# Kernel tuning notes

Hardware: AMD Instinct MI355X
Metric: run time of the kernel (lower is better)

## Reference

```python
import jax, jax.numpy as jnp
import numpy as np

DIM = 768
HEADS = 12
HEAD_DIM = DIM // HEADS
SCALE = HEAD_DIM ** -0.5


def setup_inputs() -> dict:
    key = jax.random.key(0)
    ks = jax.random.split(key, 7)
    B, N, C = 4, 1024, DIM
    s = 0.02
    return {
        "x": jax.random.normal(ks[0], (B, N, C), dtype=jnp.float32),
        "attn_mask": jax.random.normal(ks[1], (B, N, N), dtype=jnp.float32) * 0.1,
        "w_qkv": jax.random.normal(ks[2], (3 * C, C), dtype=jnp.float32) * s,
        "w_proj": jax.random.normal(ks[3], (C, C), dtype=jnp.float32) * s,
        "b_proj": jnp.zeros((C,), dtype=jnp.float32),
        "w_pre": jax.random.normal(ks[4], (HEADS, HEADS), dtype=jnp.float32) * 0.2,
        "w_post": jax.random.normal(ks[5], (HEADS, HEADS), dtype=jnp.float32) * 0.2,
    }


def reference(x, attn_mask, w_qkv, w_proj, b_proj, w_pre, w_post):
    B, N, C = x.shape
    H, D = HEADS, HEAD_DIM
    qkv = (x @ w_qkv.T).reshape(B, N, 3, H, D)
    q, k, v = jnp.moveaxis(qkv, 2, 0)          # each [B, N, H, D]
    q = q.transpose(0, 2, 1, 3)                # [B, H, N, D]
    k = k.transpose(0, 2, 1, 3)
    v = v.transpose(0, 2, 1, 3)
    attn = jnp.einsum("bhnd,bhmd->bhnm", q, k) * SCALE
    attn = attn + attn_mask[:, None, :, :]
    # talking-heads pre-softmax mixing: Linear over head axis (y = x @ W.T)
    attn = jnp.einsum("bhnm,gh->bgnm", attn, w_pre)
    attn = jax.nn.softmax(attn, axis=-1)
    # talking-heads post-softmax mixing
    attn = jnp.einsum("bhnm,gh->bgnm", attn, w_post)
    out = jnp.einsum("bhnm,bhmd->bhnd", attn, v)   # [B, H, N, D]
    out = out.transpose(0, 2, 1, 3).reshape(B, N, C)
    return out @ w_proj.T + b_proj
```

## Files before the change

kernel.cpp:

```cpp
#include <hip/hip_runtime.h>
#include <hip/hip_bf16.h>

typedef __attribute__((ext_vector_type(8))) short bf16x8;
typedef __attribute__((ext_vector_type(4))) float f32x4;
typedef unsigned short u16;

#define ATT_SCALE 0.125f

__device__ __forceinline__ u16 f2bf(float f){
  __hip_bfloat16 h = __float2bfloat16(f);
  return *reinterpret_cast<u16*>(&h);
}
__device__ __forceinline__ float bf2f(u16 u){
  __hip_bfloat16 h;
  *reinterpret_cast<u16*>(&h) = u;
  return __bfloat162float(h);
}

__global__ __launch_bounds__(256) void cvt_kernel(const float* __restrict__ src,
                                                  u16* __restrict__ dst, int n4){
  int i = blockIdx.x*256 + threadIdx.x;
  if (i < n4){
    float4 v = reinterpret_cast<const float4*>(src)[i];
    ushort4 o;
    o.x = f2bf(v.x); o.y = f2bf(v.y); o.z = f2bf(v.z); o.w = f2bf(v.w);
    reinterpret_cast<ushort4*>(dst)[i] = o;
  }
}

template<int BM, int BN, int MODE>
__global__ __launch_bounds__(256) void gemm_bt(
    const u16* __restrict__ A, const u16* __restrict__ B,
    void* __restrict__ C0, void* __restrict__ C1, void* __restrict__ C2,
    const float* __restrict__ bias,
    int M, int N, int K, int lda, int ldb, long sA, long sB, long sC)
{
  constexpr int BK = 32, LDT = 40;
  __shared__ u16 As[BM*LDT];
  __shared__ u16 Bs[BN*LDT];
  const int z = blockIdx.z;
  const u16* Ab = A + (long)z * sA;
  const u16* Bb = B + (long)z * sB;
  const int bm = blockIdx.x * BM, bn = blockIdx.y * BN;
  const int tid = threadIdx.x, lane = tid & 63, wv = tid >> 6;
  constexpr int WM = BM/2, WN = BN/2, FM = WM/16, FN = WN/16;
  const int wm = (wv >> 1) * WM, wn = (wv & 1) * WN;
  const int quad = lane >> 4, cl = lane & 15;
  f32x4 acc[FM][FN];
  #pragma unroll
  for (int i=0;i<FM;i++)
    #pragma unroll
    for (int j=0;j<FN;j++){ f32x4 zr = {0.f,0.f,0.f,0.f}; acc[i][j] = zr; }
  constexpr int AIT = (BM*BK)/(8*256);
  constexpr int BIT = (BN*BK)/(8*256);

  for (int kb = 0; kb < K; kb += BK){
    __syncthreads();
    #pragma unroll
    for (int sL=0; sL<AIT; sL++){
      int e = tid + sL*256, r = e >> 2, c8 = (e & 3) * 8;
      *reinterpret_cast<float4*>(&As[r*LDT + c8]) =
        *reinterpret_cast<const float4*>(Ab + (long)(bm + r)*lda + kb + c8);
    }
    #pragma unroll
    for (int sL=0; sL<BIT; sL++){
      int e = tid + sL*256, r = e >> 2, c8 = (e & 3) * 8;
      *reinterpret_cast<float4*>(&Bs[r*LDT + c8]) =
        *reinterpret_cast<const float4*>(Bb + (long)(bn + r)*ldb + kb + c8);
    }
    __syncthreads();
    bf16x8 af[FM], bfr[FN];
    #pragma unroll
    for (int i=0;i<FM;i++)
      af[i] = *reinterpret_cast<const bf16x8*>(&As[(wm + i*16 + cl)*LDT + quad*8]);
    #pragma unroll
    for (int j=0;j<FN;j++)
      bfr[j] = *reinterpret_cast<const bf16x8*>(&Bs[(wn + j*16 + cl)*LDT + quad*8]);
    #pragma unroll
    for (int i=0;i<FM;i++)
      #pragma unroll
      for (int j=0;j<FN;j++)
        acc[i][j] = __builtin_amdgcn_mfma_f32_16x16x32_bf16(af[i], bfr[j], acc[i][j], 0, 0, 0);
  }

  #pragma unroll
  for (int i=0;i<FM;i++)
  #pragma unroll
  for (int j=0;j<FN;j++)
  #pragma unroll
  for (int r=0;r<4;r++){
    int gm = bm + wm + i*16 + quad*4 + r;
    int gn = bn + wn + j*16 + cl;
    float v = acc[i][j][r];
    if (MODE == 0){
      int b_ = gm >> 10, n_ = gm & 1023;
      int t3 = (gn >= 1536) ? 2 : ((gn >= 768) ? 1 : 0);
      int rem = gn - t3*768;
      int h = rem >> 6, d = rem & 63;
      u16 hv = f2bf(v);
      if (t3 == 0)      ((u16*)C0)[((long)((b_*12 + h)*1024 + n_))*64 + d] = hv;
      else if (t3 == 1) ((u16*)C1)[((long)((b_*12 + h)*1024 + n_))*64 + d] = hv;
      else              ((u16*)C2)[((long)((b_*12 + h)*64 + d))*1024 + n_] = hv;
    } else if (MODE == 1){
      ((u16*)C0)[(long)z*sC + (long)gm*N + gn] = f2bf(v);
    } else if (MODE == 2){
      int b_ = z / 12, h = z - b_*12;
      ((u16*)C0)[((long)((b_*1024 + gm)*12 + h))*64 + gn] = f2bf(v);
    } else {
      ((float*)C0)[(long)gm*N + gn] = v + bias[gn];
    }
  }
}

__global__ __launch_bounds__(256) void mix_kernel(
    u16* __restrict__ S, const float* __restrict__ mask,
    const float* __restrict__ w_pre, const float* __restrict__ w_post)
{
  const int bid = blockIdx.x;
  const int b = bid >> 10, n = bid & 1023;
  const int t = threadIdx.x, wv = t >> 6, lane = t & 63;
  const int m0 = t * 4;

  float s[12][4];
  #pragma unroll
  for (int h=0; h<12; h++){
    ushort4 v = *reinterpret_cast<const ushort4*>(
        S + ((long)((b*12 + h)*1024 + n))*1024 + m0);
    s[h][0]=bf2f(v.x); s[h][1]=bf2f(v.y); s[h][2]=bf2f(v.z); s[h][3]=bf2f(v.w);
  }
  float4 mk = *reinterpret_cast<const float4*>(mask + ((long)(b*1024 + n))*1024 + m0);
  float mkv[4] = {mk.x, mk.y, mk.z, mk.w};

  float smix[12][4];
  #pragma unroll
  for (int g=0; g<12; g++){
    float rs = 0.f;
    #pragma unroll
    for (int h=0; h<12; h++) rs += w_pre[g*12 + h];
    #pragma unroll
    for (int mi=0; mi<4; mi++) smix[g][mi] = rs * mkv[mi];
    #pragma unroll
    for (int h=0; h<12; h++){
      float w = w_pre[g*12 + h] * ATT_SCALE;
      #pragma unroll
      for (int mi=0; mi<4; mi++) smix[g][mi] += w * s[h][mi];
    }
  }

  __shared__ float redA[12][4];
  __shared__ float redB[12][4];
  float Mg[12];
  #pragma unroll
  for (int g=0; g<12; g++){
    float v = fmaxf(fmaxf(smix[g][0], smix[g][1]), fmaxf(smix[g][2], smix[g][3]));
    #pragma unroll
    for (int off=32; off>0; off>>=1) v = fmaxf(v, __shfl_xor(v, off));
    if (lane == 0) redA[g][wv] = v;
  }
  __syncthreads();
  #pragma unroll
  for (int g=0; g<12; g++)
    Mg[g] = fmaxf(fmaxf(redA[g][0], redA[g][1]), fmaxf(redA[g][2], redA[g][3]));

  #pragma unroll
  for (int g=0; g<12; g++){
    float sum = 0.f;
    #pragma unroll
    for (int mi=0; mi<4; mi++){
      float e = __expf(smix[g][mi] - Mg[g]);
      smix[g][mi] = e; sum += e;
    }
    #pragma unroll
    for (int off=32; off>0; off>>=1) sum += __shfl_xor(sum, off);
    if (lane == 0) redB[g][wv] = sum;
  }
  __syncthreads();
  #pragma unroll
  for (int g=0; g<12; g++){
    float L = redB[g][0] + redB[g][1] + redB[g][2] + redB[g][3];
    float inv = 1.f / L;
    #pragma unroll
    for (int mi=0; mi<4; mi++) smix[g][mi] *= inv;
  }

  #pragma unroll
  for (int h=0; h<12; h++){
    float o0=0.f,o1=0.f,o2=0.f,o3=0.f;
    #pragma unroll
    for (int g=0; g<12; g++){
      float w = w_post[h*12 + g];
      o0 += w*smix[g][0]; o1 += w*smix[g][1]; o2 += w*smix[g][2]; o3 += w*smix[g][3];
    }
    ushort4 st; st.x=f2bf(o0); st.y=f2bf(o1); st.z=f2bf(o2); st.w=f2bf(o3);
    *reinterpret_cast<ushort4*>(S + ((long)((b*12 + h)*1024 + n))*1024 + m0) = st;
  }
}

extern "C" void kernel_launch(void* const* d_in, const int* in_sizes, int n_in,
                              void* d_out, int out_size, void* d_ws, size_t ws_size,
                              hipStream_t stream)
{
  const float* x      = (const float*)d_in[0];
  const float* mask   = (const float*)d_in[1];
  const float* w_qkv  = (const float*)d_in[2];
  const float* w_proj = (const float*)d_in[3];
  const float* b_proj = (const float*)d_in[4];
  const float* w_pre  = (const float*)d_in[5];
  const float* w_post = (const float*)d_in[6];
  float* out = (float*)d_out;

  u16* xb     = (u16*)d_ws;
  u16* wqkvb  = xb     + 4096l*768;
  u16* wprojb = wqkvb  + 2304l*768;
  u16* Qb     = wprojb + 768l*768;
  u16* Kb     = Qb     + 48l*1024*64;
  u16* Vtb    = Kb     + 48l*1024*64;
  u16* tmpb   = Vtb    + 48l*1024*64;
  u16* Sb     = tmpb   + 4096l*768;
  size_t need = ((size_t)(Sb - xb) + 48ul*1024*1024) * sizeof(u16);
  if (ws_size < need) return;

  cvt_kernel<<<(4096*768/4 + 255)/256, 256, 0, stream>>>(x,      xb,     4096*768/4);
  cvt_kernel<<<(2304*768/4 + 255)/256, 256, 0, stream>>>(w_qkv,  wqkvb,  2304*768/4);
  cvt_kernel<<<(768*768/4  + 255)/256, 256, 0, stream>>>(w_proj, wprojb, 768*768/4);

  dim3 gq(4096/128, 2304/128, 1);
  gemm_bt<128,128,0><<<gq, 256, 0, stream>>>(xb, wqkvb, Qb, Kb, Vtb, nullptr,
      4096, 2304, 768, 768, 768, 0, 0, 0);

  dim3 gs(1024/128, 1024/128, 48);
  gemm_bt<128,128,1><<<gs, 256, 0, stream>>>(Qb, Kb, Sb, nullptr, nullptr, nullptr,
      1024, 1024, 64, 64, 64, 1024l*64, 1024l*64, 1024l*1024);

  mix_kernel<<<4096, 256, 0, stream>>>(Sb, mask, w_pre, w_post);

  dim3 gp(1024/128, 1, 48);
  gemm_bt<128,64,2><<<gp, 256, 0, stream>>>(Sb, Vtb, tmpb, nullptr, nullptr, nullptr,
      1024, 64, 1024, 1024, 1024, 1024l*1024, 64l*1024, 0);

  dim3 go(4096/128, 768/128, 1);
  gemm_bt<128,128,3><<<go, 256, 0, stream>>>(tmpb, wprojb, out, nullptr, nullptr, b_proj,
      4096, 768, 768, 768, 768, 0, 0, 0);
}
```

Baseline: 275.8 us.

## Do talking-heads mixing with MFMA and drop the softmax max pass

```diff
diff --git a/kernel.cpp b/kernel.cpp
--- a/kernel.cpp
+++ b/kernel.cpp
@@ -4,6 +4,7 @@
 typedef __attribute__((ext_vector_type(8))) short bf16x8;
 typedef __attribute__((ext_vector_type(4))) float f32x4;
 typedef unsigned short u16;
+typedef unsigned int u32;
 
 #define ATT_SCALE 0.125f
 
@@ -112,87 +113,113 @@
   }
 }
 
-__global__ __launch_bounds__(256) void mix_kernel(
+#define SMP 1032
+
+__global__ __launch_bounds__(256) void mix2_kernel(
     u16* __restrict__ S, const float* __restrict__ mask,
     const float* __restrict__ w_pre, const float* __restrict__ w_post)
 {
+  __shared__ u16 Sh[12*SMP];
+  __shared__ float maskS[1024];
+  __shared__ float Lred[4][16];
+  __shared__ float LinvS[16];
+
   const int bid = blockIdx.x;
   const int b = bid >> 10, n = bid & 1023;
   const int t = threadIdx.x, wv = t >> 6, lane = t & 63;
-  const int m0 = t * 4;
-
-  float s[12][4];
-  #pragma unroll
-  for (int h=0; h<12; h++){
-    ushort4 v = *reinterpret_cast<const ushort4*>(
-        S + ((long)((b*12 + h)*1024 + n))*1024 + m0);
-    s[h][0]=bf2f(v.x); s[h][1]=bf2f(v.y); s[h][2]=bf2f(v.z); s[h][3]=bf2f(v.w);
-  }
-  float4 mk = *reinterpret_cast<const float4*>(mask + ((long)(b*1024 + n))*1024 + m0);
-  float mkv[4] = {mk.x, mk.y, mk.z, mk.w};
-
-  float smix[12][4];
-  #pragma unroll
-  for (int g=0; g<12; g++){
-    float rs = 0.f;
-    #pragma unroll
-    for (int h=0; h<12; h++) rs += w_pre[g*12 + h];
-    #pragma unroll
-    for (int mi=0; mi<4; mi++) smix[g][mi] = rs * mkv[mi];
-    #pragma unroll
-    for (int h=0; h<12; h++){
-      float w = w_pre[g*12 + h] * ATT_SCALE;
+  const int quad = lane >> 4, cl = lane & 15;
+
+  #pragma unroll
+  for (int it = 0; it < 6; it++){
+    int idx = t + it*256;
+    int h = idx >> 7, m = (idx & 127)*8;
+    *reinterpret_cast<float4*>(&Sh[h*SMP + m]) =
+      *reinterpret_cast<const float4*>(S + ((long)((b*12 + h)*1024 + n))*1024 + m);
+  }
+  for (int i = t; i < 1024; i += 256)
+    maskS[i] = mask[((long)(b*1024 + n))*1024 + i];
+
+  float rs_[4];
+  #pragma unroll
+  for (int r = 0; r < 4; r++){
+    int g = quad*4 + r;
+    float v = 0.f;
+    if (g < 12)
+      for (int h = 0; h < 12; h++) v += w_pre[g*12 + h];
+    rs_[r] = v;
+  }
+  union FragU { bf16x8 v; u32 u[4]; u16 s[8]; };
+  FragU a_pre;
+  #pragma unroll
+  for (int j = 0; j < 8; j++){
+    int k = quad*8 + j;
+    a_pre.s[j] = (cl < 12 && k < 12) ? f2bf(w_pre[cl*12 + k] * ATT_SCALE) : (u16)0;
+  }
+  __syncthreads();
+
+  u32 Ep01[16], Ep23[16];
+  float Lacc[4] = {0.f, 0.f, 0.f, 0.f};
+  const f32x4 zero4 = {0.f, 0.f, 0.f, 0.f};
+
+  #pragma unroll
+  for (int j = 0; j < 16; j++){
+    int mcol = (wv*16 + j)*16 + cl;
+    FragU bs;
+    #pragma unroll
+    for (int jj = 0; jj < 8; jj++){
+      int hh = quad*8 + jj;
+      bs.s[jj] = (hh < 12) ? Sh[hh*SMP + mcol] : (u16)0;
+    }
+    f32x4 d = __builtin_amdgcn_mfma_f32_16x16x32_bf16(a_pre.v, bs.v, zero4, 0, 0, 0);
+    float mval = maskS[mcol];
+    float e0 = __expf(d[0] + rs_[0]*mval);
+    float e1 = __expf(d[1] + rs_[1]*mval);
+    float e2 = __expf(d[2] + rs_[2]*mval);
+    float e3 = __expf(d[3] + rs_[3]*mval);
+    Lacc[0] += e0; Lacc[1] += e1; Lacc[2] += e2; Lacc[3] += e3;
+    Ep01[j] = (u32)f2bf(e0) | ((u32)f2bf(e1) << 16);
+    Ep23[j] = (u32)f2bf(e2) | ((u32)f2bf(e3) << 16);
+  }
+
+  #pragma unroll
+  for (int r = 0; r < 4; r++){
+    float v = Lacc[r];
+    v += __shfl_xor(v, 1); v += __shfl_xor(v, 2);
+    v += __shfl_xor(v, 4); v += __shfl_xor(v, 8);
+    Lacc[r] = v;
+  }
+  if (cl == 0){
+    #pragma unroll
+    for (int r = 0; r < 4; r++) Lred[wv][quad*4 + r] = Lacc[r];
+  }
+  __syncthreads();
+  if (t < 16) LinvS[t] = 1.f / (Lred[0][t] + Lred[1][t] + Lred[2][t] + Lred[3][t]);
+  __syncthreads();
+
+  FragU a_post;
+  #pragma unroll
+  for (int j = 0; j < 8; j++){
+    int k = quad*8 + j;
+    a_post.s[j] = (cl < 12 && k < 12) ? f2bf(w_post[cl*12 + k] * LinvS[k]) : (u16)0;
+  }
+
+  const int srcA = (quad << 5) + cl;
+  #pragma unroll
+  for (int j = 0; j < 16; j++){
+    int mcol = (wv*16 + j)*16 + cl;
+    FragU be;
+    be.u[0] = (u32)__shfl((int)Ep01[j], srcA, 64);
+    be.u[1] = (u32)__shfl((int)Ep23[j], srcA, 64);
+    be.u[2] = (u32)__shfl((int)Ep01[j], srcA + 16, 64);
+    be.u[3] = (u32)__shfl((int)Ep23[j], srcA + 16, 64);
+    f32x4 d = __builtin_amdgcn_mfma_f32_16x16x32_bf16(a_post.v, be.v, zero4, 0, 0, 0);
+    if (quad < 3){
       #pragma unroll
-      for (int mi=0; mi<4; mi++) smix[g][mi] += w * s[h][mi];
-    }
-  }
-
-  __shared__ float redA[12][4];
-  __shared__ float redB[12][4];
-  float Mg[12];
-  #pragma unroll
-  for (int g=0; g<12; g++){
-    float v = fmaxf(fmaxf(smix[g][0], smix[g][1]), fmaxf(smix[g][2], smix[g][3]));
-    #pragma unroll
-    for (int off=32; off>0; off>>=1) v = fmaxf(v, __shfl_xor(v, off));
-    if (lane == 0) redA[g][wv] = v;
-  }
-  __syncthreads();
-  #pragma unroll
-  for (int g=0; g<12; g++)
-    Mg[g] = fmaxf(fmaxf(redA[g][0], redA[g][1]), fmaxf(redA[g][2], redA[g][3]));
-
-  #pragma unroll
-  for (int g=0; g<12; g++){
-    float sum = 0.f;
-    #pragma unroll
-    for (int mi=0; mi<4; mi++){
-      float e = __expf(smix[g][mi] - Mg[g]);
-      smix[g][mi] = e; sum += e;
-    }
-    #pragma unroll
-    for (int off=32; off>0; off>>=1) sum += __shfl_xor(sum, off);
-    if (lane == 0) redB[g][wv] = sum;
-  }
-  __syncthreads();
-  #pragma unroll
-  for (int g=0; g<12; g++){
-    float L = redB[g][0] + redB[g][1] + redB[g][2] + redB[g][3];
-    float inv = 1.f / L;
-    #pragma unroll
-    for (int mi=0; mi<4; mi++) smix[g][mi] *= inv;
-  }
-
-  #pragma unroll
-  for (int h=0; h<12; h++){
-    float o0=0.f,o1=0.f,o2=0.f,o3=0.f;
-    #pragma unroll
-    for (int g=0; g<12; g++){
-      float w = w_post[h*12 + g];
-      o0 += w*smix[g][0]; o1 += w*smix[g][1]; o2 += w*smix[g][2]; o3 += w*smix[g][3];
-    }
-    ushort4 st; st.x=f2bf(o0); st.y=f2bf(o1); st.z=f2bf(o2); st.w=f2bf(o3);
-    *reinterpret_cast<ushort4*>(S + ((long)((b*12 + h)*1024 + n))*1024 + m0) = st;
+      for (int r = 0; r < 4; r++){
+        int h = quad*4 + r;
+        S[((long)((b*12 + h)*1024 + n))*1024 + mcol] = f2bf(d[r]);
+      }
+    }
   }
 }
 
@@ -232,7 +259,7 @@
   gemm_bt<128,128,1><<<gs, 256, 0, stream>>>(Qb, Kb, Sb, nullptr, nullptr, nullptr,
       1024, 1024, 64, 64, 64, 1024l*64, 1024l*64, 1024l*1024);
 
-  mix_kernel<<<4096, 256, 0, stream>>>(Sb, mask, w_pre, w_post);
+  mix2_kernel<<<4096, 256, 0, stream>>>(Sb, mask, w_pre, w_post);
 
   dim3 gp(1024/128, 1, 48);
   gemm_bt<128,64,2><<<gp, 256, 0, stream>>>(Sb, Vtb, tmpb, nullptr, nullptr, nullptr,
```

Measured after the change: 281.5 us. 1.02x slower.

## Fuse QK^T, pre-mix and exp, then fuse post-mix, normalize and PV

Applied to the files above, without the earlier changes.

```diff
diff --git a/kernel.cpp b/kernel.cpp
--- a/kernel.cpp
+++ b/kernel.cpp
@@ -4,6 +4,7 @@
 typedef __attribute__((ext_vector_type(8))) short bf16x8;
 typedef __attribute__((ext_vector_type(4))) float f32x4;
 typedef unsigned short u16;
+typedef unsigned int u32;
 
 #define ATT_SCALE 0.125f
 
@@ -33,14 +34,11 @@
     const u16* __restrict__ A, const u16* __restrict__ B,
     void* __restrict__ C0, void* __restrict__ C1, void* __restrict__ C2,
     const float* __restrict__ bias,
-    int M, int N, int K, int lda, int ldb, long sA, long sB, long sC)
+    int M, int N, int K, int lda, int ldb)
 {
   constexpr int BK = 32, LDT = 40;
   __shared__ u16 As[BM*LDT];
   __shared__ u16 Bs[BN*LDT];
-  const int z = blockIdx.z;
-  const u16* Ab = A + (long)z * sA;
-  const u16* Bb = B + (long)z * sB;
   const int bm = blockIdx.x * BM, bn = blockIdx.y * BN;
   const int tid = threadIdx.x, lane = tid & 63, wv = tid >> 6;
   constexpr int WM = BM/2, WN = BN/2, FM = WM/16, FN = WN/16;
@@ -60,13 +58,13 @@
     for (int sL=0; sL<AIT; sL++){
       int e = tid + sL*256, r = e >> 2, c8 = (e & 3) * 8;
       *reinterpret_cast<float4*>(&As[r*LDT + c8]) =
-        *reinterpret_cast<const float4*>(Ab + (long)(bm + r)*lda + kb + c8);
+        *reinterpret_cast<const float4*>(A + (long)(bm + r)*lda + kb + c8);
     }
     #pragma unroll
     for (int sL=0; sL<BIT; sL++){
       int e = tid + sL*256, r = e >> 2, c8 = (e & 3) * 8;
       *reinterpret_cast<float4*>(&Bs[r*LDT + c8]) =
-        *reinterpret_cast<const float4*>(Bb + (long)(bn + r)*ldb + kb + c8);
+        *reinterpret_cast<const float4*>(B + (long)(bn + r)*ldb + kb + c8);
     }
     __syncthreads();
     bf16x8 af[FM], bfr[FN];
@@ -101,98 +99,164 @@
       if (t3 == 0)      ((u16*)C0)[((long)((b_*12 + h)*1024 + n_))*64 + d] = hv;
       else if (t3 == 1) ((u16*)C1)[((long)((b_*12 + h)*1024 + n_))*64 + d] = hv;
       else              ((u16*)C2)[((long)((b_*12 + h)*64 + d))*1024 + n_] = hv;
-    } else if (MODE == 1){
-      ((u16*)C0)[(long)z*sC + (long)gm*N + gn] = f2bf(v);
-    } else if (MODE == 2){
-      int b_ = z / 12, h = z - b_*12;
-      ((u16*)C0)[((long)((b_*1024 + gm)*12 + h))*64 + gn] = f2bf(v);
     } else {
       ((float*)C0)[(long)gm*N + gn] = v + bias[gn];
     }
   }
 }
 
-__global__ __launch_bounds__(256) void mix_kernel(
-    u16* __restrict__ S, const float* __restrict__ mask,
-    const float* __restrict__ w_pre, const float* __restrict__ w_post)
+__global__ __launch_bounds__(256) void se_kernel(
+    const u16* __restrict__ Q, const u16* __restrict__ K,
+    u16* __restrict__ E, float* __restrict__ L,
+    const float* __restrict__ mask, const float* __restrict__ w_pre)
 {
-  const int bid = blockIdx.x;
-  const int b = bid >> 10, n = bid & 1023;
+  const int mt = blockIdx.x, nt = blockIdx.y, b = blockIdx.z;
   const int t = threadIdx.x, wv = t >> 6, lane = t & 63;
-  const int m0 = t * 4;
-
-  float s[12][4];
-  #pragma unroll
+  const int quad = lane >> 4, cl = lane & 15;
+  const int n0 = nt*64 + (wv >> 1)*32;
+  const int m0 = mt*32 + (wv & 1)*16;
+  const int m0c = m0 + cl;
+
+  f32x4 Dg[12][2];
+  #pragma unroll
+  for (int g=0; g<12; g++){
+    f32x4 zr = {0.f,0.f,0.f,0.f};
+    Dg[g][0] = zr; Dg[g][1] = zr;
+  }
+  const f32x4 z4 = {0.f,0.f,0.f,0.f};
+
+  #pragma unroll 2
   for (int h=0; h<12; h++){
-    ushort4 v = *reinterpret_cast<const ushort4*>(
-        S + ((long)((b*12 + h)*1024 + n))*1024 + m0);
-    s[h][0]=bf2f(v.x); s[h][1]=bf2f(v.y); s[h][2]=bf2f(v.z); s[h][3]=bf2f(v.w);
-  }
-  float4 mk = *reinterpret_cast<const float4*>(mask + ((long)(b*1024 + n))*1024 + m0);
-  float mkv[4] = {mk.x, mk.y, mk.z, mk.w};
-
-  float smix[12][4];
+    const u16* Qh = Q + ((long)(b*12 + h))*1024*64;
+    const u16* Kh = K + ((long)(b*12 + h))*1024*64;
+    bf16x8 a0  = *reinterpret_cast<const bf16x8*>(Qh + (n0      + cl)*64 + quad*8);
+    bf16x8 a0b = *reinterpret_cast<const bf16x8*>(Qh + (n0      + cl)*64 + 32 + quad*8);
+    bf16x8 a1  = *reinterpret_cast<const bf16x8*>(Qh + (n0 + 16 + cl)*64 + quad*8);
+    bf16x8 a1b = *reinterpret_cast<const bf16x8*>(Qh + (n0 + 16 + cl)*64 + 32 + quad*8);
+    bf16x8 b0  = *reinterpret_cast<const bf16x8*>(Kh + (m0      + cl)*64 + quad*8);
+    bf16x8 b0b = *reinterpret_cast<const bf16x8*>(Kh + (m0      + cl)*64 + 32 + quad*8);
+    f32x4 s0 = __builtin_amdgcn_mfma_f32_16x16x32_bf16(a0,  b0,  z4, 0, 0, 0);
+    s0       = __builtin_amdgcn_mfma_f32_16x16x32_bf16(a0b, b0b, s0, 0, 0, 0);
+    f32x4 s1 = __builtin_amdgcn_mfma_f32_16x16x32_bf16(a1,  b0,  z4, 0, 0, 0);
+    s1       = __builtin_amdgcn_mfma_f32_16x16x32_bf16(a1b, b0b, s1, 0, 0, 0);
+    #pragma unroll
+    for (int g=0; g<12; g++){
+      float w = w_pre[g*12 + h] * ATT_SCALE;
+      Dg[g][0] += s0 * w;
+      Dg[g][1] += s1 * w;
+    }
+  }
+
+  float rs[12];
   #pragma unroll
   for (int g=0; g<12; g++){
-    float rs = 0.f;
-    #pragma unroll
-    for (int h=0; h<12; h++) rs += w_pre[g*12 + h];
-    #pragma unroll
-    for (int mi=0; mi<4; mi++) smix[g][mi] = rs * mkv[mi];
-    #pragma unroll
-    for (int h=0; h<12; h++){
-      float w = w_pre[g*12 + h] * ATT_SCALE;
-      #pragma unroll
-      for (int mi=0; mi<4; mi++) smix[g][mi] += w * s[h][mi];
-    }
-  }
-
-  __shared__ float redA[12][4];
-  __shared__ float redB[12][4];
-  float Mg[12];
-  #pragma unroll
-  for (int g=0; g<12; g++){
-    float v = fmaxf(fmaxf(smix[g][0], smix[g][1]), fmaxf(smix[g][2], smix[g][3]));
-    #pragma unroll
-    for (int off=32; off>0; off>>=1) v = fmaxf(v, __shfl_xor(v, off));
-    if (lane == 0) redA[g][wv] = v;
+    float v = 0.f;
+    #pragma unroll
+    for (int h=0; h<12; h++) v += w_pre[g*12 + h];
+    rs[g] = v;
+  }
+
+  #pragma unroll
+  for (int f=0; f<2; f++)
+  #pragma unroll
+  for (int r=0; r<4; r++){
+    int n = n0 + f*16 + quad*4 + r;
+    float mv = mask[((long)(b*1024 + n))*1024 + m0c];
+    #pragma unroll
+    for (int g=0; g<12; g++){
+      float e = __expf(Dg[g][f][r] + rs[g]*mv);
+      E[((long)((b*12 + g)*1024 + n))*1024 + m0c] = f2bf(e);
+      float v = e;
+      v += __shfl_xor(v, 1); v += __shfl_xor(v, 2);
+      v += __shfl_xor(v, 4); v += __shfl_xor(v, 8);
+      if (cl == 0) atomicAdd(&L[(b*12 + g)*1024 + n], v);
+    }
+  }
+}
+
+__global__ __launch_bounds__(512) void pv_kernel(
+    const u16* __restrict__ E, const u16* __restrict__ Vt,
+    const float* __restrict__ L, u16* __restrict__ tmp,
+    const float* __restrict__ w_post)
+{
+  __shared__ float red[4*64*52];
+  const int nt = blockIdx.x, b = blockIdx.y;
+  const int t = threadIdx.x, wv = t >> 6, lane = t & 63;
+  const int quad = lane >> 4, cl = lane & 15;
+  const int hset = wv >> 1, mp = wv & 1;
+  const int n0 = nt*16;
+
+  float invL[12];
+  #pragma unroll
+  for (int g=0; g<12; g++)
+    invL[g] = 1.0f / L[(b*12 + g)*1024 + n0 + cl];
+
+  f32x4 O[3][4];
+  #pragma unroll
+  for (int hh=0; hh<3; hh++)
+    #pragma unroll
+    for (int df=0; df<4; df++){ f32x4 zr = {0.f,0.f,0.f,0.f}; O[hh][df] = zr; }
+
+  for (int c = mp*16; c < mp*16 + 16; c++){
+    const long m0 = (long)c*32 + quad*8;
+    float P[3][8];
+    #pragma unroll
+    for (int hh=0; hh<3; hh++)
+      #pragma unroll
+      for (int j=0; j<8; j++) P[hh][j] = 0.f;
+
+    #pragma unroll
+    for (int g=0; g<12; g++){
+      union { bf16x8 v; u16 s[8]; } ef;
+      ef.v = *reinterpret_cast<const bf16x8*>(
+          E + ((long)((b*12 + g)*1024 + n0 + cl))*1024 + m0);
+      #pragma unroll
+      for (int j=0; j<8; j++){
+        float en = bf2f(ef.s[j]) * invL[g];
+        #pragma unroll
+        for (int hh=0; hh<3; hh++)
+          P[hh][j] += w_post[(hset*3 + hh)*12 + g] * en;
+      }
+    }
+    #pragma unroll
+    for (int hh=0; hh<3; hh++){
+      int h = hset*3 + hh;
+      union { bf16x8 v; u16 s[8]; } pa;
+      #pragma unroll
+      for (int j=0; j<8; j++) pa.s[j] = f2bf(P[hh][j]);
+      #pragma unroll
+      for (int df=0; df<4; df++){
+        bf16x8 vb = *reinterpret_cast<const bf16x8*>(
+            Vt + ((long)((b*12 + h)*64 + df*16 + cl))*1024 + m0);
+        O[hh][df] = __builtin_amdgcn_mfma_f32_16x16x32_bf16(pa.v, vb, O[hh][df], 0, 0, 0);
+      }
+    }
+  }
+
+  if (mp == 1){
+    float* base = red + (hset*64 + lane)*52;
+    #pragma unroll
+    for (int hh=0; hh<3; hh++)
+      #pragma unroll
+      for (int df=0; df<4; df++)
+        *reinterpret_cast<f32x4*>(base + (hh*4 + df)*4) = O[hh][df];
   }
   __syncthreads();
-  #pragma unroll
-  for (int g=0; g<12; g++)
-    Mg[g] = fmaxf(fmaxf(redA[g][0], redA[g][1]), fmaxf(redA[g][2], redA[g][3]));
-
-  #pragma unroll
-  for (int g=0; g<12; g++){
-    float sum = 0.f;
-    #pragma unroll
-    for (int mi=0; mi<4; mi++){
-      float e = __expf(smix[g][mi] - Mg[g]);
-      smix[g][mi] = e; sum += e;
-    }
-    #pragma unroll
-    for (int off=32; off>0; off>>=1) sum += __shfl_xor(sum, off);
-    if (lane == 0) redB[g][wv] = sum;
-  }
-  __syncthreads();
-  #pragma unroll
-  for (int g=0; g<12; g++){
-    float L = redB[g][0] + redB[g][1] + redB[g][2] + redB[g][3];
-    float inv = 1.f / L;
-    #pragma unroll
-    for (int mi=0; mi<4; mi++) smix[g][mi] *= inv;
-  }
-
-  #pragma unroll
-  for (int h=0; h<12; h++){
-    float o0=0.f,o1=0.f,o2=0.f,o3=0.f;
-    #pragma unroll
-    for (int g=0; g<12; g++){
-      float w = w_post[h*12 + g];
-      o0 += w*smix[g][0]; o1 += w*smix[g][1]; o2 += w*smix[g][2]; o3 += w*smix[g][3];
-    }
-    ushort4 st; st.x=f2bf(o0); st.y=f2bf(o1); st.z=f2bf(o2); st.w=f2bf(o3);
-    *reinterpret_cast<ushort4*>(S + ((long)((b*12 + h)*1024 + n))*1024 + m0) = st;
+  if (mp == 0){
+    const float* base = red + (hset*64 + lane)*52;
+    #pragma unroll
+    for (int hh=0; hh<3; hh++){
+      int h = hset*3 + hh;
+      #pragma unroll
+      for (int df=0; df<4; df++){
+        f32x4 o = O[hh][df] + *reinterpret_cast<const f32x4*>(base + (hh*4 + df)*4);
+        #pragma unroll
+        for (int r=0; r<4; r++){
+          int n = n0 + quad*4 + r;
+          tmp[((long)(b*1024 + n))*768 + h*64 + df*16 + cl] = f2bf(o[r]);
+        }
+      }
+    }
   }
 }
 
@@ -215,10 +279,13 @@
   u16* Qb     = wprojb + 768l*768;
   u16* Kb     = Qb     + 48l*1024*64;
   u16* Vtb    = Kb     + 48l*1024*64;
-  u16* tmpb   = Vtb    + 48l*1024*64;
-  u16* Sb     = tmpb   + 4096l*768;
-  size_t need = ((size_t)(Sb - xb) + 48ul*1024*1024) * sizeof(u16);
+  u16* Eb     = Vtb    + 48l*1024*64;
+  float* Lf   = (float*)(Eb + 48l*1024*1024);
+  u16* tmpb   = xb;
+  size_t need = ((size_t)((u16*)Lf - xb) + 2ul*48*1024) * sizeof(u16);
   if (ws_size < need) return;
+
+  hipMemsetAsync(Lf, 0, 48l*1024*sizeof(float), stream);
 
   cvt_kernel<<<(4096*768/4 + 255)/256, 256, 0, stream>>>(x,      xb,     4096*768/4);
   cvt_kernel<<<(2304*768/4 + 255)/256, 256, 0, stream>>>(w_qkv,  wqkvb,  2304*768/4);
@@ -226,19 +293,15 @@
 
   dim3 gq(4096/128, 2304/128, 1);
   gemm_bt<128,128,0><<<gq, 256, 0, stream>>>(xb, wqkvb, Qb, Kb, Vtb, nullptr,
-      4096, 2304, 768, 768, 768, 0, 0, 0);
-
-  dim3 gs(1024/128, 1024/128, 48);
-  gemm_bt<128,128,1><<<gs, 256, 0, stream>>>(Qb, Kb, Sb, nullptr, nullptr, nullptr,
-      1024, 1024, 64, 64, 64, 1024l*64, 1024l*64, 1024l*1024);
-
-  mix_kernel<<<4096, 256, 0, stream>>>(Sb, mask, w_pre, w_post);
-
-  dim3 gp(1024/128, 1, 48);
-  gemm_bt<128,64,2><<<gp, 256, 0, stream>>>(Sb, Vtb, tmpb, nullptr, nullptr, nullptr,
-      1024, 64, 1024, 1024, 1024, 1024l*1024, 64l*1024, 0);
+      4096, 2304, 768, 768, 768);
+
+  dim3 gse(32, 16, 4);
+  se_kernel<<<gse, 256, 0, stream>>>(Qb, Kb, Eb, Lf, mask, w_pre);
+
+  dim3 gpv(64, 4);
+  pv_kernel<<<gpv, 512, 0, stream>>>(Eb, Vtb, Lf, tmpb, w_post);
 
   dim3 go(4096/128, 768/128, 1);
   gemm_bt<128,128,3><<<go, 256, 0, stream>>>(tmpb, wprojb, out, nullptr, nullptr, b_proj,
-      4096, 768, 768, 768, 768, 0, 0, 0);
-}
+      4096, 768, 768, 768, 768);
+}
```

After: 453.9 us. 64.5% more time.
